# Performance work log

Measured on AMD Instinct MI355X. Metric: run time of the kernel, lower is better.

The kernel has to match this reference:

```python
import jax, jax.numpy as jnp
import numpy as np

NEG_INF = -1.0e9
LN_EPS = 1e-5
LEAK = 0.2


def setup_inputs() -> dict:
    key = jax.random.key(0)
    ks = jax.random.split(key, 8)
    B, C, T, N, H = 8, 64, 24, 512, 2
    hd = C // H
    x = jax.random.normal(ks[0], (B, C, T, N), dtype=jnp.float32)
    gso = jax.random.randint(ks[1], (N, N), 0, 2, dtype=jnp.int32)
    # torch nn.Linear weights are (out, in); xavier-ish scale
    s = (2.0 / (C + C)) ** 0.5
    Wq = jax.random.normal(ks[2], (C, C), dtype=jnp.float32) * s
    Wk = jax.random.normal(ks[3], (C, C), dtype=jnp.float32) * s
    Wv = jax.random.normal(ks[4], (C, C), dtype=jnp.float32) * s
    sa = (2.0 / (H + hd)) ** 0.5
    a_src = jax.random.normal(ks[5], (H, hd), dtype=jnp.float32) * sa
    a_dst = jax.random.normal(ks[6], (H, hd), dtype=jnp.float32) * sa
    ln_gamma = jnp.ones((C,), dtype=jnp.float32)
    ln_beta = jnp.zeros((C,), dtype=jnp.float32)
    return {"x": x, "gso": gso, "Wq": Wq, "Wk": Wk, "Wv": Wv,
            "a_src": a_src, "a_dst": a_dst, "ln_gamma": ln_gamma, "ln_beta": ln_beta}


def _spatial_gat(x, gso, Wq, Wk, Wv, a_src, a_dst, ln_gamma, ln_beta):
    B, C, T, N = x.shape
    H, hd = a_src.shape
    # (B, C, T, N) -> (B*T, N, C)
    xr = jnp.transpose(x, (0, 2, 3, 1)).reshape(B * T, N, C)
    # torch Linear: y = x @ W.T
    Q = jnp.einsum('bnc,dc->bnd', xr, Wq).reshape(B * T, N, H, hd)
    K = jnp.einsum('bnc,dc->bnd', xr, Wk).reshape(B * T, N, H, hd)
    V = jnp.einsum('bnc,dc->bnd', xr, Wv).reshape(B * T, N, H, hd)
    # additive GAT scores, all heads at once
    s_src = jnp.einsum('bnhd,hd->bnh', Q, a_src)  # (BT, N, H)
    s_dst = jnp.einsum('bnhd,hd->bnh', K, a_dst)  # (BT, N, H)
    scores = jax.nn.leaky_relu(s_src[:, :, None, :] + s_dst[:, None, :, :], LEAK)  # (BT, Ni, Nj, H)
    mask = jnp.where(gso == 0, jnp.float32(NEG_INF), jnp.float32(0.0))  # (N, N)
    scores = scores + mask[None, :, :, None]
    attn = jax.nn.softmax(scores, axis=2)  # softmax over destination j
    out = jnp.einsum('bijh,bjhd->bihd', attn, V)  # (BT, N, H, hd)
    out = out.reshape(B * T, N, C)
    # LayerNorm over channel dim
    mu = jnp.mean(out, axis=-1, keepdims=True)
    var = jnp.var(out, axis=-1, keepdims=True)
    out = (out - mu) * jax.lax.rsqrt(var + LN_EPS) * ln_gamma + ln_beta
    # back to (B, C, T, N)
    return jnp.transpose(out.reshape(B, T, N, C), (0, 3, 1, 2))


def reference(x, gso, Wq, Wk, Wv, a_src, a_dst, ln_gamma, ln_beta):
    return _spatial_gat(x, gso, Wq, Wk, Wv, a_src, a_dst, ln_gamma, ln_beta)
```

## Files before the change

kernel.cpp:

```cpp
#include <hip/hip_runtime.h>

#define CDIM 64
#define TDIM 24
#define NDIM 512
#define NBT  192

typedef float    float4v __attribute__((ext_vector_type(4)));
typedef _Float16 half8v  __attribute__((ext_vector_type(8)));
typedef _Float16 half4v  __attribute__((ext_vector_type(4)));
typedef _Float16 half2v  __attribute__((ext_vector_type(2)));


__device__ __forceinline__ float exp2_fast(float x) {
#if __has_builtin(__builtin_amdgcn_exp2f)
  return __builtin_amdgcn_exp2f(x);
#else
  return __expf(x * 0.69314718f);
#endif
}

__device__ __forceinline__ half2v pk2(float a, float b) {
  return __builtin_bit_cast(half2v, __builtin_amdgcn_cvt_pkrtz(a, b));
}

struct SmemK1 {
  union {
    _Float16 xt[128][72];
    _Float16 vtb[64][136];
  } big;
  _Float16 wv[64][72];
  _Float16 wext[16][72];
};

__launch_bounds__(256, 4)
__global__ void k1_v(const float* __restrict__ x,  const float* __restrict__ Wv,
                     const float* __restrict__ Wq, const float* __restrict__ Wk,
                     const float* __restrict__ a_src, const float* __restrict__ a_dst,
                     const int* __restrict__ gso,
                     _Float16* __restrict__ VT_g,
                     float* __restrict__ s_src_g, float* __restrict__ s_dst_g,
                     unsigned short* __restrict__ mask16) {
  const int t  = threadIdx.x;
  const int bx = blockIdx.x;

  if (bx >= 768) {
    int g = (bx - 768) * 256 + t;
    const int4* gp = (const int4*)gso + (size_t)g * 4;
    unsigned w[8];
#pragma unroll
    for (int k = 0; k < 4; ++k) {
      int4 v = gp[k];
      w[2 * k]     = (v.x ? 0x0000FFFFu : 0u) | (v.y ? 0xFFFF0000u : 0u);
      w[2 * k + 1] = (v.z ? 0x0000FFFFu : 0u) | (v.w ? 0xFFFF0000u : 0u);
    }
    uint4 o0; o0.x = w[0]; o0.y = w[1]; o0.z = w[2]; o0.w = w[3];
    uint4 o1; o1.x = w[4]; o1.y = w[5]; o1.z = w[6]; o1.w = w[7];
    ((uint4*)mask16)[g * 2]     = o0;
    ((uint4*)mask16)[g * 2 + 1] = o1;
    return;
  }

  __shared__ SmemK1 sm;
  const int qn = bx & 3;
  const int bt = bx >> 2;
  const int b  = bt / TDIM, tt = bt % TDIM;
  const int n0 = qn * 128;

#pragma unroll
  for (int it = 0; it < 4; ++it) {
    int idx = it * 256 + t;
    int d = idx >> 4, k4 = (idx & 15) * 4;
    float4 v = ((const float4*)Wv)[idx];
    half2v p0 = pk2(v.x, v.y), p1 = pk2(v.z, v.w);
    half4v h4; h4[0] = p0[0]; h4[1] = p0[1]; h4[2] = p1[0]; h4[3] = p1[1];
    *(half4v*)&sm.wv[d][k4] = h4;
  }
  for (int z = t; z < 12 * 72; z += 256) ((_Float16*)sm.wext[4])[z] = (_Float16)0.f;
  {
    int r = t >> 6, c = t & 63;
    const float* av = (r & 2) ? a_dst : a_src;
    const float* W  = (r & 2) ? Wk : Wq;
    int off = (r & 1) * 32;
    float s = 0.f;
#pragma unroll
    for (int d = 0; d < 32; ++d)
      s += av[off + d] * W[(off + d) * 64 + c];
    sm.wext[r][c] = (_Float16)(s * 1.44269504f);
  }
  for (int it = 0; it < 16; ++it) {
    int idx = it * 256 + t;
    int cp = idx >> 7, n = idx & 127;
    int c0 = cp * 2;
    const float* base = x + ((size_t)(b * CDIM + c0) * TDIM + tt) * NDIM + n0 + n;
    *(half2v*)&sm.big.xt[n][c0] = pk2(base[0], base[(size_t)TDIM * NDIM]);
  }
  __syncthreads();

  const int lane = t & 63, w = t >> 6;
  const int m = lane & 15, quad = lane >> 4;
  const int mbase = w * 32;

  float4v acc[2][5];
#pragma unroll
  for (int mt = 0; mt < 2; ++mt)
#pragma unroll
    for (int nt = 0; nt < 5; ++nt)
#pragma unroll
      for (int r = 0; r < 4; ++r) acc[mt][nt][r] = 0.f;

#pragma unroll
  for (int ks = 0; ks < 2; ++ks) {
    half8v af[2], bf[5];
#pragma unroll
    for (int mt = 0; mt < 2; ++mt)
      af[mt] = *(const half8v*)&sm.big.xt[mbase + mt * 16 + m][ks * 32 + quad * 8];
#pragma unroll
    for (int nt = 0; nt < 4; ++nt)
      bf[nt] = *(const half8v*)&sm.wv[nt * 16 + m][ks * 32 + quad * 8];
    bf[4] = *(const half8v*)&sm.wext[m][ks * 32 + quad * 8];
#pragma unroll
    for (int mt = 0; mt < 2; ++mt)
#pragma unroll
      for (int nt = 0; nt < 5; ++nt)
        acc[mt][nt] = __builtin_amdgcn_mfma_f32_16x16x32_f16(af[mt], bf[nt], acc[mt][nt], 0, 0, 0);
  }

  if (m < 4) {
    float* basep = (m < 2 ? s_src_g : s_dst_g) + (size_t)(bt * 2 + (m & 1)) * NDIM;
#pragma unroll
    for (int mt = 0; mt < 2; ++mt)
#pragma unroll
      for (int r = 0; r < 4; ++r)
        basep[n0 + mbase + mt * 16 + quad * 4 + r] = acc[mt][4][r];
  }
  __syncthreads();

#pragma unroll
  for (int mt = 0; mt < 2; ++mt)
#pragma unroll
    for (int nt = 0; nt < 4; ++nt)
#pragma unroll
      for (int r = 0; r < 4; r += 2) {
        int nl = mbase + mt * 16 + quad * 4 + r;
        int c  = nt * 16 + m;
        *(half2v*)&sm.big.vtb[c][nl] = pk2(acc[mt][nt][r], acc[mt][nt][r + 1]);
      }
  __syncthreads();

  const unsigned* vdw = (const unsigned*)sm.big.vtb;
  unsigned* outdw = (unsigned*)VT_g;
  for (int it = 0; it < 16; ++it) {
    int idx = it * 256 + t;
    int c = idx >> 6, jd = idx & 63;
    outdw[(size_t)(bt * 64 + c) * 256 + qn * 64 + jd] = vdw[c * 68 + jd];
  }
}

struct SmemK2 {
  union {
    struct { _Float16 vt[64][128]; unsigned short mb[64][136]; } s;
    struct { float otile[64][66]; float rsum[4][64]; float rsq[4][64];
             float mu[64]; float rs[64]; } e;
  } u;
  _Float16 sF16[2][512];
  _Float16 sP16[2][512];
};

__launch_bounds__(256, 4)
__global__ void k2_attn(const _Float16* __restrict__ VT_g,
                        const float* __restrict__ s_src_g, const float* __restrict__ s_dst_g,
                        const unsigned short* __restrict__ mask16,
                        const float* __restrict__ gamma, const float* __restrict__ beta,
                        float* __restrict__ out) {
  __shared__ SmemK2 sm;
  const int t     = threadIdx.x;
  const int itile = blockIdx.x;
  const int bt    = blockIdx.y;
  const int i0    = itile * 64;
  const int b     = bt / TDIM, tt = bt % TDIM;
  const int lane  = t & 63, w = t >> 6;
  const int h = w >> 1, ihalf = w & 1;
  const int m = lane & 15, quad = lane >> 4;

  for (int it = 0; it < 4; ++it) {
    int idx = it * 256 + t;
    float d = s_dst_g[(size_t)bt * 2 * NDIM + idx];
    ((_Float16*)sm.sF16)[idx] = (_Float16)exp2_fast(d);
    ((_Float16*)sm.sP16)[idx] = (_Float16)exp2_fast(0.2f * d);
  }
  half8v E8[2], Q8[2];
#pragma unroll
  for (int mt = 0; mt < 2; ++mt) {
    float sv = s_src_g[(size_t)(bt * 2 + h) * NDIM + i0 + ihalf * 32 + mt * 16 + m];
    _Float16 ev = (_Float16)exp2_fast(sv - 6.f);
    _Float16 qv = (_Float16)exp2_fast(0.2f * sv - 6.f);
#pragma unroll
    for (int jj = 0; jj < 8; ++jj) { E8[mt][jj] = ev; Q8[mt][jj] = qv; }
  }

  float4v acc[2][2], accs[2];
#pragma unroll
  for (int mt = 0; mt < 2; ++mt) {
#pragma unroll
    for (int r = 0; r < 4; ++r) { acc[mt][0][r] = 0.f; acc[mt][1][r] = 0.f; accs[mt][r] = 0.f; }
  }
  const half8v bones = {(_Float16)1.f, (_Float16)1.f, (_Float16)1.f, (_Float16)1.f,
                        (_Float16)1.f, (_Float16)1.f, (_Float16)1.f, (_Float16)1.f};

  for (int js = 0; js < 4; ++js) {
    __syncthreads();
    {
      const uint4* vsrc = (const uint4*)VT_g;
#pragma unroll
      for (int it = 0; it < 4; ++it) {
        int idx = it * 256 + t;
        int c = idx >> 4, ch = idx & 15;
        uint4 val = vsrc[(size_t)(bt * 64 + c) * 64 + js * 16 + ch];
        *(uint4*)&sm.u.s.vt[c][(ch * 8) ^ ((c & 7) * 8)] = val;
      }
      const uint4* msrc = (const uint4*)mask16;
#pragma unroll
      for (int it = 0; it < 4; ++it) {
        int idx = it * 256 + t;
        int c = idx >> 4, ch = idx & 15;
        uint4 mv = msrc[(size_t)(i0 + c) * 64 + js * 16 + ch];
        *(uint4*)&sm.u.s.mb[c][ch * 8] = mv;
      }
    }
    __syncthreads();

#pragma unroll
    for (int ksl = 0; ksl < 4; ++ksl) {
      int jq = ksl * 32 + quad * 8;
      half8v F8 = *(const half8v*)&sm.sF16[h][js * 128 + jq];
      half8v P8 = *(const half8v*)&sm.sP16[h][js * 128 + jq];
      int vbase = (h * 32 + m) * 128 + (jq ^ ((m & 7) * 8));
      half8v b0 = *(const half8v*)&sm.u.s.vt[0][vbase];
      half8v b1 = *(const half8v*)&sm.u.s.vt[0][vbase + 16 * 128];
#pragma unroll
      for (int mt = 0; mt < 2; ++mt) {
        uint4 mv = *(const uint4*)&sm.u.s.mb[ihalf * 32 + mt * 16 + m][jq];
        half8v e8 = __builtin_elementwise_max(E8[mt] * F8, Q8[mt] * P8);
        uint4 eu = __builtin_bit_cast(uint4, e8);
        eu.x &= mv.x; eu.y &= mv.y; eu.z &= mv.z; eu.w &= mv.w;
        half8v af = __builtin_bit_cast(half8v, eu);
        acc[mt][0] = __builtin_amdgcn_mfma_f32_16x16x32_f16(af, b0,    acc[mt][0], 0, 0, 0);
        acc[mt][1] = __builtin_amdgcn_mfma_f32_16x16x32_f16(af, b1,    acc[mt][1], 0, 0, 0);
        accs[mt]   = __builtin_amdgcn_mfma_f32_16x16x32_f16(af, bones, accs[mt],   0, 0, 0);
      }
    }
  }

  __syncthreads();
#pragma unroll
  for (int mt = 0; mt < 2; ++mt)
#pragma unroll
    for (int r = 0; r < 4; ++r) {
      float sc = __builtin_amdgcn_rcpf(accs[mt][r]);
      int i_loc = ihalf * 32 + mt * 16 + quad * 4 + r;
#pragma unroll
      for (int nt = 0; nt < 2; ++nt)
        sm.u.e.otile[i_loc][h * 32 + nt * 16 + m] = acc[mt][nt][r] * sc;
    }
  __syncthreads();

  {
    int i = t & 63, cg = t >> 6;
    float s1 = 0.f, s2 = 0.f;
#pragma unroll
    for (int cc = 0; cc < 16; ++cc) {
      float v = sm.u.e.otile[i][cg * 16 + cc];
      s1 += v; s2 += v * v;
    }
    sm.u.e.rsum[cg][i] = s1;
    sm.u.e.rsq[cg][i]  = s2;
  }
  __syncthreads();
  if (t < 64) {
    int i = t;
    float s1 = 0.f, s2 = 0.f;
#pragma unroll
    for (int cg = 0; cg < 4; ++cg) { s1 += sm.u.e.rsum[cg][i]; s2 += sm.u.e.rsq[cg][i]; }
    float mu  = s1 * (1.f / 64.f);
    float var = s2 * (1.f / 64.f) - mu * mu;
    sm.u.e.mu[i] = mu;
    sm.u.e.rs[i] = rsqrtf(var + 1e-5f);
  }
  __syncthreads();
  {
    int i = t & 63, cg = t >> 6;
    float mu = sm.u.e.mu[i], rs = sm.u.e.rs[i];
    int n = i0 + i;
#pragma unroll
    for (int cc = 0; cc < 16; ++cc) {
      int c = cg * 16 + cc;
      float v = (sm.u.e.otile[i][c] - mu) * rs * gamma[c] + beta[c];
      out[((size_t)(b * CDIM + c) * TDIM + tt) * NDIM + n] = v;
    }
  }
}

extern "C" void kernel_launch(void* const* d_in, const int* in_sizes, int n_in,
                              void* d_out, int out_size, void* d_ws, size_t ws_size,
                              hipStream_t stream) {
  const float* x     = (const float*)d_in[0];
  const int*   gso   = (const int*)d_in[1];
  const float* Wq    = (const float*)d_in[2];
  const float* Wk    = (const float*)d_in[3];
  const float* Wv    = (const float*)d_in[4];
  const float* a_src = (const float*)d_in[5];
  const float* a_dst = (const float*)d_in[6];
  const float* gamma = (const float*)d_in[7];
  const float* beta  = (const float*)d_in[8];
  float* out = (float*)d_out;

  char* ws = (char*)d_ws;
  _Float16* VT_g  = (_Float16*)ws;
  float*    s_src = (float*)(ws + 12582912);
  float*    s_dst = (float*)(ws + 13369344);
  unsigned short* mask16 = (unsigned short*)(ws + 14155776);

  k1_v<<<832, 256, 0, stream>>>(x, Wv, Wq, Wk, a_src, a_dst, gso,
                                VT_g, s_src, s_dst, mask16);
  k2_attn<<<dim3(8, NBT), 256, 0, stream>>>(VT_g, s_src, s_dst, mask16, gamma, beta, out);
}
```

Baseline: 138.3 us.

## Load V and byte mask directly from global in attention loop, drop LDS staging

The mask is now stored as one byte per entry instead of 16-bit, halving its footprint, and is expanded to 16-bit lane masks in registers with byte-permute instructions. The attention kernel no longer stages V and mask tiles through shared memory with two barriers per step; each lane reads its MFMA B operand and mask bytes straight from global memory. This removes the LDS round trips and syncs and shrinks LDS use, at the cost of less coalesced global reads that rely on cache reuse across blocks.

```diff
diff --git a/kernel.cpp b/kernel.cpp
--- a/kernel.cpp
+++ b/kernel.cpp
@@ -39,24 +39,22 @@
                      const int* __restrict__ gso,
                      _Float16* __restrict__ VT_g,
                      float* __restrict__ s_src_g, float* __restrict__ s_dst_g,
-                     unsigned short* __restrict__ mask16) {
+                     unsigned char* __restrict__ maskb) {
   const int t  = threadIdx.x;
   const int bx = blockIdx.x;
 
   if (bx >= 768) {
     int g = (bx - 768) * 256 + t;
     const int4* gp = (const int4*)gso + (size_t)g * 4;
-    unsigned w[8];
+    unsigned w[4];
 #pragma unroll
     for (int k = 0; k < 4; ++k) {
       int4 v = gp[k];
-      w[2 * k]     = (v.x ? 0x0000FFFFu : 0u) | (v.y ? 0xFFFF0000u : 0u);
-      w[2 * k + 1] = (v.z ? 0x0000FFFFu : 0u) | (v.w ? 0xFFFF0000u : 0u);
-    }
-    uint4 o0; o0.x = w[0]; o0.y = w[1]; o0.z = w[2]; o0.w = w[3];
-    uint4 o1; o1.x = w[4]; o1.y = w[5]; o1.z = w[6]; o1.w = w[7];
-    ((uint4*)mask16)[g * 2]     = o0;
-    ((uint4*)mask16)[g * 2 + 1] = o1;
+      w[k] = (v.x ? 0x000000FFu : 0u) | (v.y ? 0x0000FF00u : 0u) |
+             (v.z ? 0x00FF0000u : 0u) | (v.w ? 0xFF000000u : 0u);
+    }
+    uint4 o; o.x = w[0]; o.y = w[1]; o.z = w[2]; o.w = w[3];
+    ((uint4*)maskb)[g] = o;
     return;
   }
 
@@ -157,11 +155,10 @@
 }
 
 struct SmemK2 {
-  union {
-    struct { _Float16 vt[64][128]; unsigned short mb[64][136]; } s;
-    struct { float otile[64][66]; float rsum[4][64]; float rsq[4][64];
-             float mu[64]; float rs[64]; } e;
-  } u;
+  float otile[64][66];
+  float rsum[4][64];
+  float rsq[4][64];
+  float mu[64], rs[64];
   _Float16 sF16[2][512];
   _Float16 sP16[2][512];
 };
@@ -169,7 +166,7 @@
 __launch_bounds__(256, 4)
 __global__ void k2_attn(const _Float16* __restrict__ VT_g,
                         const float* __restrict__ s_src_g, const float* __restrict__ s_dst_g,
-                        const unsigned short* __restrict__ mask16,
+                        const unsigned char* __restrict__ maskb,
                         const float* __restrict__ gamma, const float* __restrict__ beta,
                         float* __restrict__ out) {
   __shared__ SmemK2 sm;
@@ -207,42 +204,31 @@
   const half8v bones = {(_Float16)1.f, (_Float16)1.f, (_Float16)1.f, (_Float16)1.f,
                         (_Float16)1.f, (_Float16)1.f, (_Float16)1.f, (_Float16)1.f};
 
+  const _Float16* vrow = VT_g + ((size_t)bt * 64 + h * 32 + m) * NDIM;
+  const unsigned char* mrow0 = maskb + (size_t)(i0 + ihalf * 32 + m) * NDIM;
+  const unsigned char* mrow1 = mrow0 + 16 * NDIM;
+
+  __syncthreads();
+
   for (int js = 0; js < 4; ++js) {
-    __syncthreads();
-    {
-      const uint4* vsrc = (const uint4*)VT_g;
-#pragma unroll
-      for (int it = 0; it < 4; ++it) {
-        int idx = it * 256 + t;
-        int c = idx >> 4, ch = idx & 15;
-        uint4 val = vsrc[(size_t)(bt * 64 + c) * 64 + js * 16 + ch];
-        *(uint4*)&sm.u.s.vt[c][(ch * 8) ^ ((c & 7) * 8)] = val;
-      }
-      const uint4* msrc = (const uint4*)mask16;
-#pragma unroll
-      for (int it = 0; it < 4; ++it) {
-        int idx = it * 256 + t;
-        int c = idx >> 4, ch = idx & 15;
-        uint4 mv = msrc[(size_t)(i0 + c) * 64 + js * 16 + ch];
-        *(uint4*)&sm.u.s.mb[c][ch * 8] = mv;
-      }
-    }
-    __syncthreads();
-
 #pragma unroll
     for (int ksl = 0; ksl < 4; ++ksl) {
-      int jq = ksl * 32 + quad * 8;
-      half8v F8 = *(const half8v*)&sm.sF16[h][js * 128 + jq];
-      half8v P8 = *(const half8v*)&sm.sP16[h][js * 128 + jq];
-      int vbase = (h * 32 + m) * 128 + (jq ^ ((m & 7) * 8));
-      half8v b0 = *(const half8v*)&sm.u.s.vt[0][vbase];
-      half8v b1 = *(const half8v*)&sm.u.s.vt[0][vbase + 16 * 128];
+      int jo = js * 128 + ksl * 32 + quad * 8;
+      half8v b0 = *(const half8v*)(vrow + jo);
+      half8v b1 = *(const half8v*)(vrow + 16 * NDIM + jo);
+      uint2 mv0 = *(const uint2*)(mrow0 + jo);
+      uint2 mv1 = *(const uint2*)(mrow1 + jo);
+      half8v F8 = *(const half8v*)&sm.sF16[h][jo];
+      half8v P8 = *(const half8v*)&sm.sP16[h][jo];
 #pragma unroll
       for (int mt = 0; mt < 2; ++mt) {
-        uint4 mv = *(const uint4*)&sm.u.s.mb[ihalf * 32 + mt * 16 + m][jq];
+        uint2 mv = mt ? mv1 : mv0;
         half8v e8 = __builtin_elementwise_max(E8[mt] * F8, Q8[mt] * P8);
         uint4 eu = __builtin_bit_cast(uint4, e8);
-        eu.x &= mv.x; eu.y &= mv.y; eu.z &= mv.z; eu.w &= mv.w;
+        eu.x &= __builtin_amdgcn_perm(0u, mv.x, 0x01010000u);
+        eu.y &= __builtin_amdgcn_perm(0u, mv.x, 0x03030202u);
+        eu.z &= __builtin_amdgcn_perm(0u, mv.y, 0x01010000u);
+        eu.w &= __builtin_amdgcn_perm(0u, mv.y, 0x03030202u);
         half8v af = __builtin_bit_cast(half8v, eu);
         acc[mt][0] = __builtin_amdgcn_mfma_f32_16x16x32_f16(af, b0,    acc[mt][0], 0, 0, 0);
         acc[mt][1] = __builtin_amdgcn_mfma_f32_16x16x32_f16(af, b1,    acc[mt][1], 0, 0, 0);
@@ -251,7 +237,6 @@
     }
   }
 
-  __syncthreads();
 #pragma unroll
   for (int mt = 0; mt < 2; ++mt)
 #pragma unroll
@@ -260,7 +245,7 @@
       int i_loc = ihalf * 32 + mt * 16 + quad * 4 + r;
 #pragma unroll
       for (int nt = 0; nt < 2; ++nt)
-        sm.u.e.otile[i_loc][h * 32 + nt * 16 + m] = acc[mt][nt][r] * sc;
+        sm.otile[i_loc][h * 32 + nt * 16 + m] = acc[mt][nt][r] * sc;
     }
   __syncthreads();
 
@@ -269,32 +254,32 @@
     float s1 = 0.f, s2 = 0.f;
 #pragma unroll
     for (int cc = 0; cc < 16; ++cc) {
-      float v = sm.u.e.otile[i][cg * 16 + cc];
+      float v = sm.otile[i][cg * 16 + cc];
       s1 += v; s2 += v * v;
     }
-    sm.u.e.rsum[cg][i] = s1;
-    sm.u.e.rsq[cg][i]  = s2;
+    sm.rsum[cg][i] = s1;
+    sm.rsq[cg][i]  = s2;
   }
   __syncthreads();
   if (t < 64) {
     int i = t;
     float s1 = 0.f, s2 = 0.f;
 #pragma unroll
-    for (int cg = 0; cg < 4; ++cg) { s1 += sm.u.e.rsum[cg][i]; s2 += sm.u.e.rsq[cg][i]; }
+    for (int cg = 0; cg < 4; ++cg) { s1 += sm.rsum[cg][i]; s2 += sm.rsq[cg][i]; }
     float mu  = s1 * (1.f / 64.f);
     float var = s2 * (1.f / 64.f) - mu * mu;
-    sm.u.e.mu[i] = mu;
-    sm.u.e.rs[i] = rsqrtf(var + 1e-5f);
+    sm.mu[i] = mu;
+    sm.rs[i] = rsqrtf(var + 1e-5f);
   }
   __syncthreads();
   {
     int i = t & 63, cg = t >> 6;
-    float mu = sm.u.e.mu[i], rs = sm.u.e.rs[i];
+    float mu = sm.mu[i], rs = sm.rs[i];
     int n = i0 + i;
 #pragma unroll
     for (int cc = 0; cc < 16; ++cc) {
       int c = cg * 16 + cc;
-      float v = (sm.u.e.otile[i][c] - mu) * rs * gamma[c] + beta[c];
+      float v = (sm.otile[i][c] - mu) * rs * gamma[c] + beta[c];
       out[((size_t)(b * CDIM + c) * TDIM + tt) * NDIM + n] = v;
     }
   }
@@ -318,9 +303,9 @@
   _Float16* VT_g  = (_Float16*)ws;
   float*    s_src = (float*)(ws + 12582912);
   float*    s_dst = (float*)(ws + 13369344);
-  unsigned short* mask16 = (unsigned short*)(ws + 14155776);
+  unsigned char* maskb = (unsigned char*)(ws + 14155776);
 
   k1_v<<<832, 256, 0, stream>>>(x, Wv, Wq, Wk, a_src, a_dst, gso,
-                                VT_g, s_src, s_dst, mask16);
-  k2_attn<<<dim3(8, NBT), 256, 0, stream>>>(VT_g, s_src, s_dst, mask16, gamma, beta, out);
-}
+                                VT_g, s_src, s_dst, maskb);
+  k2_attn<<<dim3(8, NBT), 256, 0, stream>>>(VT_g, s_src, s_dst, maskb, gamma, beta, out);
+}
```

After: 139.8 us. No clear change (+1.1%).
